# Performance work log

Hardware: AMD Instinct MI355X
Metric: run time of the kernel (lower is better)

The kernel has to match this reference:

```python
import jax, jax.numpy as jnp
import numpy as np

B = 131072
IN_DIM = 310   # 300 + zdimension_Gap(10)
H1 = 128       # g_neural_network_width
D = 100        # hard-coded data_t / generate_data width
SLOPE = 0.01   # torch LeakyReLU default negative_slope


def _leaky(v):
    return jnp.where(v >= 0, v, SLOPE * v)


def setup_inputs() -> dict:
    key = jax.random.key(0)
    ks = jax.random.split(key, 8)
    # kaiming_normal fan_in, a=0: std = sqrt(2 / fan_in)
    W1 = jax.random.normal(ks[0], (IN_DIM, 10), jnp.float32) * np.sqrt(2.0 / IN_DIM)
    b1 = jnp.zeros((10,), jnp.float32)
    W2 = jax.random.normal(ks[1], (10, H1), jnp.float32) * np.sqrt(2.0 / 10)
    b2 = jnp.zeros((H1,), jnp.float32)
    W3 = jax.random.normal(ks[2], (H1, 2), jnp.float32) * np.sqrt(2.0 / H1)
    b3 = jnp.zeros((2,), jnp.float32)
    x = jax.random.normal(ks[3], (B, IN_DIM), jnp.float32)
    data_t = jax.random.normal(ks[4], (B, D), jnp.float32)
    return {"x": x, "data_t": data_t, "W1": W1, "b1": b1,
            "W2": W2, "b2": b2, "W3": W3, "b3": b3}


def reference(x, data_t, W1, b1, W2, b2, W3, b3):
    # 3-layer MLP with LeakyReLU -> coeff [B, 2]
    h = _leaky(x @ W1 + b1)
    h = _leaky(h @ W2 + b2)
    coeff = _leaky(h @ W3 + b3)
    # polynomial basis: only power-1 (data_t) and power-2 (data_t**2) terms are used
    t2 = data_t * data_t  # [B, D]
    # generate_data[i] = coeff[i,0]*data_t[i] + coeff[i,1]*data_t[i]**2 (vectorized over batch)
    generate_data = coeff[:, 0:1] * data_t + coeff[:, 1:2] * t2
    return generate_data
```

## Files before the change

### kernel.cpp

```cpp
#include <hip/hip_runtime.h>
#include <stdint.h>

typedef float f32x2 __attribute__((ext_vector_type(2)));
typedef float f32x4 __attribute__((ext_vector_type(4)));

#define TILE_F 19840
#define NTPB   4
#define PSTR   84
#define CP_OFF 5376
#define CPSTR  20
#define LDSF   (TILE_F + 128)
#define LDS_BYTES (LDSF * 4)

__device__ __forceinline__ float leaky(float v) { return fmaxf(v, 0.01f * v); }
__device__ __forceinline__ f32x2 leaky2(f32x2 v) {
    return __builtin_elementwise_max(v, v * 0.01f);
}

template<int KQ>
__device__ __forceinline__ void l1_fma(const float* xr, const float* __restrict__ Wb,
                                       float* acc) {
    #pragma unroll
    for (int q = 0; q < (KQ + 7) / 8; ++q) {
        f32x2 xp[4];
        #pragma unroll
        for (int i = 0; i < 4; ++i)
            if (q * 8 + 2 * i < KQ) xp[i] = *(const f32x2*)(xr + q * 8 + 2 * i);
        #pragma unroll
        for (int k = 0; k < 8; ++k) {
            if (q * 8 + k < KQ) {
                const float xs = (k & 1) ? xp[k >> 1].y : xp[k >> 1].x;
                #pragma unroll
                for (int j = 0; j < 10; ++j)
                    acc[j] = fmaf(xs, Wb[(q * 8 + k) * 10 + j], acc[j]);
            }
        }
    }
}

__global__ __launch_bounds__(512, 4) void gen_mlp_r9(
    const float* __restrict__ x, const float* __restrict__ data_t,
    const float* __restrict__ W1, const float* __restrict__ b1,
    const float* __restrict__ W2, const float* __restrict__ b2,
    const float* __restrict__ W3, const float* __restrict__ b3,
    float* __restrict__ out)
{
    extern __shared__ float lds[];
    float* buf = lds;
    float* ccs = lds + TILE_F;

    const int t    = threadIdx.x;
    const int lane = t & 63;
    const int row  = lane;
    const int wq   = __builtin_amdgcn_readfirstlane(t >> 6);

    const int tile0 = blockIdx.x * NTPB;

    {
        const float* g = x + (size_t)tile0 * TILE_F;
        #pragma unroll
        for (int i = 0; i < 10; ++i) {
            const int gi = i * 2048 + t * 4;
            if (gi < TILE_F) *(f32x4*)(buf + gi) = *(const f32x4*)(g + gi);
        }
    }
    asm volatile("s_waitcnt lgkmcnt(0)" ::: "memory");
    __builtin_amdgcn_s_barrier();

    #pragma unroll 1
    for (int it = 0; it < NTPB; ++it) {
        const int tile = tile0 + it;
        const bool pf  = (it + 1 < NTPB);

        f32x4 px[10];
        {
            const float* gn = x + (size_t)(tile + 1) * TILE_F;
            #pragma unroll
            for (int i = 0; i < 10; ++i) {
                const int gi = i * 2048 + t * 4;
                if (pf && gi < TILE_F) px[i] = *(const f32x4*)(gn + gi);
            }
        }

        float acc[10] = {0,0,0,0,0,0,0,0,0,0};
        const float* xr = buf + row * 310 + wq * 40;
        if (wq == 7) l1_fma<30>(xr, W1 + 2800, acc);
        else         l1_fma<40>(xr, W1 + wq * 400, acc);

        asm volatile("s_waitcnt lgkmcnt(0)" ::: "memory");
        __builtin_amdgcn_s_barrier();

        {
            float* pw = buf + row * PSTR + wq * 10;
            #pragma unroll
            for (int j = 0; j < 5; ++j)
                *(f32x2*)(pw + 2 * j) = (f32x2){acc[2 * j], acc[2 * j + 1]};
        }
        asm volatile("s_waitcnt lgkmcnt(0)" ::: "memory");
        __builtin_amdgcn_s_barrier();

        const f32x4* dt4 = (const f32x4*)data_t + (size_t)tile * 1600;
        f32x4 tv0 = dt4[t], tv1 = dt4[512 + t], tv2 = dt4[1024 + t], tv3;
        if (t < 64) tv3 = dt4[1536 + t];

        float h1[10];
        {
            const float* pr = buf + row * PSTR;
            float s[10];
            #pragma unroll
            for (int j = 0; j < 10; ++j) s[j] = b1[j];
            #pragma unroll
            for (int sl = 0; sl < 8; ++sl) {
                #pragma unroll
                for (int m = 0; m < 5; ++m) {
                    f32x2 v = *(const f32x2*)(pr + sl * 10 + 2 * m);
                    s[2 * m]     += v.x;
                    s[2 * m + 1] += v.y;
                }
            }
            #pragma unroll
            for (int j = 0; j < 10; ++j) h1[j] = leaky(s[j]);
        }

        float hh[16];
        #pragma unroll
        for (int jj = 0; jj < 16; ++jj) hh[jj] = b2[wq * 16 + jj];
        #pragma unroll
        for (int k = 0; k < 10; ++k) {
            #pragma unroll
            for (int jj = 0; jj < 16; ++jj)
                hh[jj] = fmaf(h1[k], W2[k * 128 + wq * 16 + jj], hh[jj]);
        }
        f32x2 p = {0.f, 0.f};
        #pragma unroll
        for (int jj = 0; jj < 16; ++jj) {
            const float s = leaky(hh[jj]);
            p.x = fmaf(s, W3[(wq * 16 + jj) * 2 + 0], p.x);
            p.y = fmaf(s, W3[(wq * 16 + jj) * 2 + 1], p.y);
        }

        *(f32x2*)(buf + CP_OFF + row * CPSTR + 2 * wq) = p;
        asm volatile("s_waitcnt lgkmcnt(0)" ::: "memory");
        __builtin_amdgcn_s_barrier();

        if (wq == 0) {
            const float* cb = buf + CP_OFF + row * CPSTR;
            f32x2 q = {b3[0], b3[1]};
            #pragma unroll
            for (int i = 0; i < 4; ++i) {
                f32x4 v = *(const f32x4*)(cb + 4 * i);
                q.x += v[0] + v[2];
                q.y += v[1] + v[3];
            }
            *(f32x2*)(ccs + 2 * row) = leaky2(q);
        }
        asm volatile("s_waitcnt lgkmcnt(0)" ::: "memory");
        __builtin_amdgcn_s_barrier();

        if (pf) {
            #pragma unroll
            for (int i = 0; i < 10; ++i) {
                const int gi = i * 2048 + t * 4;
                if (gi < TILE_F) *(f32x4*)(buf + gi) = px[i];
            }
        }
        asm volatile("s_waitcnt lgkmcnt(0)" ::: "memory");
        __builtin_amdgcn_s_barrier();

        f32x4* o4 = (f32x4*)out + (size_t)tile * 1600;
        {
            f32x2 cc = *(const f32x2*)(ccs + 2 * (t / 25) * 0 + 2 * ((0 * 512 + t) / 25));
            (void)cc;
        }
        #pragma unroll
        for (int i = 0; i < 3; ++i) {
            const int idx = i * 512 + t;
            f32x2 cc = *(const f32x2*)(ccs + 2 * (idx / 25));
            f32x4 tt = (i == 0) ? tv0 : (i == 1) ? tv1 : tv2;
            o4[idx] = tt * (tt * cc.y + cc.x);
        }
        if (t < 64) {
            const int idx = 1536 + t;
            f32x2 cc = *(const f32x2*)(ccs + 2 * (idx / 25));
            o4[idx] = tv3 * (tv3 * cc.y + cc.x);
        }
    }
}

extern "C" void kernel_launch(void* const* d_in, const int* in_sizes, int n_in,
                              void* d_out, int out_size, void* d_ws, size_t ws_size,
                              hipStream_t stream) {
    const float* x      = (const float*)d_in[0];
    const float* data_t = (const float*)d_in[1];
    const float* W1     = (const float*)d_in[2];
    const float* b1     = (const float*)d_in[3];
    const float* W2     = (const float*)d_in[4];
    const float* b2     = (const float*)d_in[5];
    const float* W3     = (const float*)d_in[6];
    const float* b3     = (const float*)d_in[7];
    float* out = (float*)d_out;

    hipFuncSetAttribute((const void*)gen_mlp_r9,
                        hipFuncAttributeMaxDynamicSharedMemorySize, LDS_BYTES);
    gen_mlp_r9<<<512, 512, LDS_BYTES, stream>>>(x, data_t, W1, b1, W2, b2, W3, b3, out);
}
```

Before: 59.79 us.

## Prefetch next x tile directly into LDS with global_load_lds in two regions

Replaces the register-staged prefetch of the next 64-row x tile with direct global-to-LDS loads, split into a front region (A) and a back region (B). Each is issued once that part of the buffer is no longer needed: B right after the layer-1 inputs are copied to registers, A after the scratch partial sums are consumed. The layer-1 inputs are now pulled into 40 registers before the barrier, and the partial-sum and coeff scratch strides are compacted to fit inside region A. This frees the 40 prefetch registers and removes one barrier plus the LDS store pass, at the cost of a tricky vmcnt-based wait whose count must cover the outstanding output stores.

Result: slower. 76.41 us (+27.8%).

```diff
diff --git a/kernel.cpp b/kernel.cpp
--- a/kernel.cpp
+++ b/kernel.cpp
@@ -6,9 +6,12 @@
 
 #define TILE_F 19840
 #define NTPB   4
-#define PSTR   84
-#define CP_OFF 5376
-#define CPSTR  20
+#define PSTR   80
+#define CP_OFF 5120
+#define CPSTR  16
+#define A_F    6144
+#define BPW    1712
+#define APW    768
 #define LDSF   (TILE_F + 128)
 #define LDS_BYTES (LDSF * 4)
 
@@ -17,28 +20,36 @@
     return __builtin_elementwise_max(v, v * 0.01f);
 }
 
+__device__ __forceinline__ void gload16(const float* g, float* l) {
+    auto gp = reinterpret_cast<const float __attribute__((address_space(1)))*>(
+        reinterpret_cast<uintptr_t>(g));
+    auto lp = reinterpret_cast<float __attribute__((address_space(3)))*>(
+        reinterpret_cast<uintptr_t>(l));
+    __builtin_amdgcn_global_load_lds(gp, lp, 16, 0, 0);
+}
+
+__device__ __forceinline__ void stage_B(const float* src, float* dst, int lane) {
+    #pragma unroll
+    for (int i = 0; i < 6; ++i) gload16(src + i * 256, dst + i * 256);
+    if (lane < 44) gload16(src + 6 * 256, dst + 6 * 256);
+}
+__device__ __forceinline__ void stage_A(const float* src, float* dst) {
+    #pragma unroll
+    for (int i = 0; i < 3; ++i) gload16(src + i * 256, dst + i * 256);
+}
+
 template<int KQ>
-__device__ __forceinline__ void l1_fma(const float* xr, const float* __restrict__ Wb,
+__device__ __forceinline__ void fma_xk(const float* xk, const float* __restrict__ Wb,
                                        float* acc) {
     #pragma unroll
-    for (int q = 0; q < (KQ + 7) / 8; ++q) {
-        f32x2 xp[4];
-        #pragma unroll
-        for (int i = 0; i < 4; ++i)
-            if (q * 8 + 2 * i < KQ) xp[i] = *(const f32x2*)(xr + q * 8 + 2 * i);
-        #pragma unroll
-        for (int k = 0; k < 8; ++k) {
-            if (q * 8 + k < KQ) {
-                const float xs = (k & 1) ? xp[k >> 1].y : xp[k >> 1].x;
-                #pragma unroll
-                for (int j = 0; j < 10; ++j)
-                    acc[j] = fmaf(xs, Wb[(q * 8 + k) * 10 + j], acc[j]);
-            }
-        }
+    for (int k = 0; k < KQ; ++k) {
+        #pragma unroll
+        for (int j = 0; j < 10; ++j)
+            acc[j] = fmaf(xk[k], Wb[k * 10 + j], acc[j]);
     }
 }
 
-__global__ __launch_bounds__(512, 4) void gen_mlp_r9(
+__global__ __launch_bounds__(512, 4) void gen_mlp_r12(
     const float* __restrict__ x, const float* __restrict__ data_t,
     const float* __restrict__ W1, const float* __restrict__ b1,
     const float* __restrict__ W2, const float* __restrict__ b2,
@@ -58,50 +69,52 @@
 
     {
         const float* g = x + (size_t)tile0 * TILE_F;
-        #pragma unroll
-        for (int i = 0; i < 10; ++i) {
-            const int gi = i * 2048 + t * 4;
-            if (gi < TILE_F) *(f32x4*)(buf + gi) = *(const f32x4*)(g + gi);
-        }
+        stage_A(g + wq * APW + lane * 4,       buf + wq * APW);
+        stage_B(g + A_F + wq * BPW + lane * 4, buf + A_F + wq * BPW, lane);
     }
-    asm volatile("s_waitcnt lgkmcnt(0)" ::: "memory");
+    asm volatile("s_waitcnt vmcnt(0)" ::: "memory");
     __builtin_amdgcn_s_barrier();
 
     #pragma unroll 1
     for (int it = 0; it < NTPB; ++it) {
         const int tile = tile0 + it;
         const bool pf  = (it + 1 < NTPB);
-
-        f32x4 px[10];
-        {
-            const float* gn = x + (size_t)(tile + 1) * TILE_F;
-            #pragma unroll
-            for (int i = 0; i < 10; ++i) {
-                const int gi = i * 2048 + t * 4;
-                if (pf && gi < TILE_F) px[i] = *(const f32x4*)(gn + gi);
-            }
-        }
-
-        float acc[10] = {0,0,0,0,0,0,0,0,0,0};
-        const float* xr = buf + row * 310 + wq * 40;
-        if (wq == 7) l1_fma<30>(xr, W1 + 2800, acc);
-        else         l1_fma<40>(xr, W1 + wq * 400, acc);
-
-        asm volatile("s_waitcnt lgkmcnt(0)" ::: "memory");
-        __builtin_amdgcn_s_barrier();
-
-        {
-            float* pw = buf + row * PSTR + wq * 10;
-            #pragma unroll
-            for (int j = 0; j < 5; ++j)
-                *(f32x2*)(pw + 2 * j) = (f32x2){acc[2 * j], acc[2 * j + 1]};
-        }
-        asm volatile("s_waitcnt lgkmcnt(0)" ::: "memory");
-        __builtin_amdgcn_s_barrier();
+        const float* gnext = x + (size_t)(tile + 1) * TILE_F;
 
         const f32x4* dt4 = (const f32x4*)data_t + (size_t)tile * 1600;
         f32x4 tv0 = dt4[t], tv1 = dt4[512 + t], tv2 = dt4[1024 + t], tv3;
         if (t < 64) tv3 = dt4[1536 + t];
+
+        float xk[40];
+        {
+            const float* xr = buf + row * 310 + wq * 40;
+            if (wq == 7) {
+                #pragma unroll
+                for (int q = 0; q < 15; ++q)
+                    *(f32x2*)&xk[2 * q] = *(const f32x2*)(xr + 2 * q);
+            } else {
+                #pragma unroll
+                for (int q = 0; q < 20; ++q)
+                    *(f32x2*)&xk[2 * q] = *(const f32x2*)(xr + 2 * q);
+            }
+        }
+        asm volatile("s_waitcnt lgkmcnt(0)" ::: "memory");
+        __builtin_amdgcn_s_barrier();
+
+        if (pf) stage_B(gnext + A_F + wq * BPW + lane * 4, buf + A_F + wq * BPW, lane);
+
+        float acc[10] = {0,0,0,0,0,0,0,0,0,0};
+        if (wq == 7) fma_xk<30>(xk, W1 + 2800, acc);
+        else         fma_xk<40>(xk, W1 + wq * 400, acc);
+
+        {
+            float* pw = buf + row * PSTR + wq * 10;
+            #pragma unroll
+            for (int j = 0; j < 5; ++j)
+                *(f32x2*)(pw + 2 * j) = (f32x2){acc[2 * j], acc[2 * j + 1]};
+        }
+        asm volatile("s_waitcnt lgkmcnt(0)" ::: "memory");
+        __builtin_amdgcn_s_barrier();
 
         float h1[10];
         {
@@ -157,32 +170,32 @@
         asm volatile("s_waitcnt lgkmcnt(0)" ::: "memory");
         __builtin_amdgcn_s_barrier();
 
-        if (pf) {
-            #pragma unroll
-            for (int i = 0; i < 10; ++i) {
-                const int gi = i * 2048 + t * 4;
-                if (gi < TILE_F) *(f32x4*)(buf + gi) = px[i];
-            }
-        }
-        asm volatile("s_waitcnt lgkmcnt(0)" ::: "memory");
-        __builtin_amdgcn_s_barrier();
+        if (pf) stage_A(gnext + wq * APW + lane * 4, buf + wq * APW);
 
         f32x4* o4 = (f32x4*)out + (size_t)tile * 1600;
         {
-            f32x2 cc = *(const f32x2*)(ccs + 2 * (t / 25) * 0 + 2 * ((0 * 512 + t) / 25));
-            (void)cc;
-        }
-        #pragma unroll
-        for (int i = 0; i < 3; ++i) {
-            const int idx = i * 512 + t;
+            f32x2 cc = *(const f32x2*)(ccs + 2 * (t / 25));
+            o4[t] = tv0 * (tv0 * cc.y + cc.x);
+        }
+        {
+            const int idx = 512 + t;
             f32x2 cc = *(const f32x2*)(ccs + 2 * (idx / 25));
-            f32x4 tt = (i == 0) ? tv0 : (i == 1) ? tv1 : tv2;
-            o4[idx] = tt * (tt * cc.y + cc.x);
+            o4[idx] = tv1 * (tv1 * cc.y + cc.x);
+        }
+        {
+            const int idx = 1024 + t;
+            f32x2 cc = *(const f32x2*)(ccs + 2 * (idx / 25));
+            o4[idx] = tv2 * (tv2 * cc.y + cc.x);
         }
         if (t < 64) {
             const int idx = 1536 + t;
             f32x2 cc = *(const f32x2*)(ccs + 2 * (idx / 25));
             o4[idx] = tv3 * (tv3 * cc.y + cc.x);
+        }
+
+        if (pf) {
+            asm volatile("s_waitcnt vmcnt(4)" ::: "memory");
+            __builtin_amdgcn_s_barrier();
         }
     }
 }
@@ -200,7 +213,7 @@
     const float* b3     = (const float*)d_in[7];
     float* out = (float*)d_out;
 
-    hipFuncSetAttribute((const void*)gen_mlp_r9,
+    hipFuncSetAttribute((const void*)gen_mlp_r12,
                         hipFuncAttributeMaxDynamicSharedMemorySize, LDS_BYTES);
-    gen_mlp_r9<<<512, 512, LDS_BYTES, stream>>>(x, data_t, W1, b1, W2, b2, W3, b3, out);
-}
+    gen_mlp_r12<<<512, 512, LDS_BYTES, stream>>>(x, data_t, W1, b1, W2, b2, W3, b3, out);
+}
```
